# Kernel optimization log

Measured on AMD Instinct MI355X. Metric: run time of the kernel, lower is better.

The kernel has to match this reference:

```python
import jax, jax.numpy as jnp
import numpy as np

PATCHES = 196
HEADS = 12


def build_attention_mask(patches, memory_tokens_list, extension=False):
    """Additive mask: masked entries -inf, allowed entries 0. Shape (1, Sq, Skv)."""
    class_tokens = len(memory_tokens_list) + 1
    input_tokens = patches + class_tokens
    total_tokens = input_tokens + sum(memory_tokens_list)
    mask = np.zeros((1, input_tokens, total_tokens), dtype=np.float32)
    mask[:, :, patches + 1:] = -np.inf
    prev = 0
    for i, mtok in enumerate(memory_tokens_list):
        ct = patches + 1 + i
        ms = input_tokens + prev
        me = ms + mtok
        if extension:
            mask[:, ct:, ct] = 0.0
            mask[:, ct:, ms:me] = 0.0
        else:
            mask[:, ct, ct] = 0.0
            mask[:, ct, ms:me] = 0.0
        prev += mtok
    return mask


def setup_inputs() -> dict:
    key = jax.random.key(0)
    ks = jax.random.split(key, 5)
    B, Sq, D, M = 64, PATCHES + 2, 768, 8  # 1 base class token + 1 memory class token
    std = 0.02
    return {
        "hidden_states": jax.random.normal(ks[0], (B, Sq, D), jnp.float32),
        "memory": jax.random.normal(ks[1], (1, M, D), jnp.float32) * std,
        "Wq": jax.random.normal(ks[2], (D, D), jnp.float32) * std,
        "bq": jnp.zeros((D,), jnp.float32),
        "Wk": jax.random.normal(ks[3], (D, D), jnp.float32) * std,
        "bk": jnp.zeros((D,), jnp.float32),
        "Wv": jax.random.normal(ks[4], (D, D), jnp.float32) * std,
        "bv": jnp.zeros((D,), jnp.float32),
    }


def _split_heads(x, heads):
    B, S, D = x.shape
    return x.reshape(B, S, heads, D // heads)  # bshd


def reference(hidden_states, memory, Wq, bq, Wk, bk, Wv, bv):
    B, Sq, D = hidden_states.shape
    M = memory.shape[1]
    head_dim = D // HEADS
    scale = 1.0 / jnp.sqrt(jnp.asarray(head_dim, hidden_states.dtype))
    # static additive mask (1, Sq, Skv)
    mask = jnp.asarray(build_attention_mask(PATCHES, [M]))

    with_memory = jnp.concatenate(
        [hidden_states, jnp.broadcast_to(memory, (B, M, D))], axis=1)  # (B, Skv, D)

    q = _split_heads(hidden_states @ Wq + bq, HEADS)  # (B,Sq,H,dh)
    k = _split_heads(with_memory @ Wk + bk, HEADS)    # (B,Skv,H,dh)
    v = _split_heads(with_memory @ Wv + bv, HEADS)

    scores = jnp.einsum("bqhd,bkhd->bhqk", q, k) * scale + mask[:, None]  # (B,H,Sq,Skv)
    probs = jax.nn.softmax(scores, axis=-1)  # dropout is identity in eval
    ctx = jnp.einsum("bhqk,bkhd->bqhd", probs, v)
    return ctx.reshape(B, Sq, D)
```

## Files before the change

kernel.cpp:

```cpp
#include <hip/hip_runtime.h>

typedef __attribute__((ext_vector_type(8))) short bf16x8;
typedef __attribute__((ext_vector_type(4))) float f32x4;
typedef __attribute__((ext_vector_type(4))) unsigned int u32x4;

#define NB 64
#define SQ 198
#define SKV 206
#define DM 768
#define NH 12
#define NROWS (NB * SKV)
#define NCOL 2304

static __device__ __forceinline__ unsigned short f2b(float f) {
  union { float f; unsigned u; } v; v.f = f;
  unsigned r = v.u + 0x7FFFu + ((v.u >> 16) & 1u);
  return (unsigned short)(r >> 16);
}

typedef const __attribute__((address_space(1))) unsigned int g_u32;
typedef __attribute__((address_space(3))) unsigned int l_u32;
static __device__ __forceinline__ void gload_lds16(const void* g, void* l) {
  __builtin_amdgcn_global_load_lds((g_u32*)g, (l_u32*)l, 16, 0, 0);
}

__global__ __launch_bounds__(256) void k_conv_x(const float* __restrict__ hid,
                                                const float* __restrict__ mem,
                                                unsigned short* __restrict__ xkv) {
  int idx = (blockIdx.x * 256 + threadIdx.x) * 8;
  int r = idx / DM;
  int c = idx - r * DM;
  int b = r / SKV, s = r - b * SKV;
  const float* src = (s < SQ) ? (hid + (b * SQ + s) * DM + c)
                              : (mem + (s - SQ) * DM + c);
  float4 v0 = ((const float4*)src)[0];
  float4 v1 = ((const float4*)src)[1];
  unsigned w0 = f2b(v0.x) | ((unsigned)f2b(v0.y) << 16);
  unsigned w1 = f2b(v0.z) | ((unsigned)f2b(v0.w) << 16);
  unsigned w2 = f2b(v1.x) | ((unsigned)f2b(v1.y) << 16);
  unsigned w3 = f2b(v1.z) | ((unsigned)f2b(v1.w) << 16);
  u32x4 o = {w0, w1, w2, w3};
  *(u32x4*)(xkv + idx) = o;
}

__global__ __launch_bounds__(256) void k_conv_w(const float* __restrict__ Wq,
                                                const float* __restrict__ Wk,
                                                const float* __restrict__ Wv,
                                                unsigned short* __restrict__ wt) {
  __shared__ float L[64][65];
  int w = blockIdx.z;
  int n0 = blockIdx.x * 64, k0 = blockIdx.y * 64;
  const float* W = (w == 0) ? Wq : (w == 1) ? Wk : Wv;
  int tid = threadIdx.x;
#pragma unroll
  for (int i = 0; i < 16; ++i) {
    int idx = i * 256 + tid;
    int lr = idx >> 6, lc = idx & 63;
    L[lr][lc] = W[(k0 + lr) * DM + n0 + lc];
  }
  __syncthreads();
  unsigned short* dst = wt + w * DM * DM;
#pragma unroll
  for (int o = 0; o < 2; ++o) {
    int gi = o * 256 + tid;
    int rn = gi >> 3, g = gi & 7;
    unsigned wrd[4];
#pragma unroll
    for (int jj = 0; jj < 4; ++jj) {
      float f0 = L[g * 8 + jj * 2 + 0][rn];
      float f1 = L[g * 8 + jj * 2 + 1][rn];
      wrd[jj] = f2b(f0) | ((unsigned)f2b(f1) << 16);
    }
    u32x4 o4 = {wrd[0], wrd[1], wrd[2], wrd[3]};
    *(u32x4*)(dst + (n0 + rn) * DM + k0 + g * 8) = o4;
  }
}

__global__ __launch_bounds__(512, 4) void k_gemm(const unsigned short* __restrict__ xkv,
                                                 const unsigned short* __restrict__ wt,
                                                 const float* __restrict__ bq,
                                                 const float* __restrict__ bk,
                                                 const float* __restrict__ bv,
                                                 unsigned short* __restrict__ cout) {
  __shared__ __align__(16) unsigned char smem[73728];
  int o = blockIdx.x, xcd = o & 7, rest = o >> 3;
  int sid = (xcd < 7 ? xcd * 116 : 812) + (xcd < 7 ? 0 : (xcd - 7) * 115) + rest;
  int mtile = sid / 9, ntile = sid - mtile * 9;
  int row0 = mtile * 128, col0 = ntile * 256;
  int w = ntile / 3;
  int colw0 = (ntile - w * 3) * 256;
  int tid = threadIdx.x, lane = tid & 63, wid = tid >> 6;
  int wm = wid >> 2, wn = wid & 3;
  int l = lane & 15, gq = lane >> 4;
  const unsigned short* wbase = wt + w * DM * DM;

  const unsigned short* aP;
  const unsigned short* bP0;
  const unsigned short* bP1;
  {
    int sr = tid >> 2, pg = tid & 3, sg = pg ^ ((sr >> 1) & 3);
    aP  = xkv   + (row0 + sr) * DM + sg * 8;
    bP0 = wbase + (colw0 + sr) * DM + sg * 8;
    bP1 = wbase + (colw0 + 128 + sr) * DM + sg * 8;
  }
  int ldsW = wid * 1024;

  f32x4 zero = {0.f, 0.f, 0.f, 0.f};
  f32x4 acc[4][4];
#pragma unroll
  for (int i = 0; i < 4; ++i)
#pragma unroll
    for (int j = 0; j < 4; ++j) acc[i][j] = zero;

#pragma unroll
  for (int p = 0; p < 2; ++p) {
    int bo = p * 24576;
    gload_lds16(aP  + p * 32, smem + bo + ldsW);
    gload_lds16(bP0 + p * 32, smem + bo + 8192 + ldsW);
    gload_lds16(bP1 + p * 32, smem + bo + 16384 + ldsW);
  }
  asm volatile("s_waitcnt vmcnt(3)" ::: "memory");
  __builtin_amdgcn_s_barrier();

  int swx = (gq * 16) ^ (((l >> 1) & 3) << 4);
  int aRd = (wm * 64 + l) * 64 + swx;
  int bRd = 8192 + (wn * 64 + l) * 64 + swx;

  int q = 0;
  int qn = 2;
#pragma unroll 1
  for (int t = 0; t < 24; ++t) {
    const unsigned char* bp = smem + q * 24576;
    if (t < 22) {
      unsigned char* ip = smem + qn * 24576;
      int kI = (t + 2) * 32;
      gload_lds16(aP  + kI, ip + ldsW);
      gload_lds16(bP0 + kI, ip + 8192 + ldsW);
      gload_lds16(bP1 + kI, ip + 16384 + ldsW);
    }
    bf16x8 a[4], b[4];
#pragma unroll
    for (int mi = 0; mi < 4; ++mi) a[mi] = *(const bf16x8*)(bp + aRd + mi * 1024);
#pragma unroll
    for (int ni = 0; ni < 4; ++ni) b[ni] = *(const bf16x8*)(bp + bRd + ni * 1024);
    __builtin_amdgcn_s_setprio(1);
#pragma unroll
    for (int mi = 0; mi < 4; ++mi)
#pragma unroll
      for (int ni = 0; ni < 4; ++ni)
        acc[mi][ni] = __builtin_amdgcn_mfma_f32_16x16x32_bf16(a[mi], b[ni], acc[mi][ni], 0, 0, 0);
    __builtin_amdgcn_s_setprio(0);
    if (t < 22)       { asm volatile("s_waitcnt vmcnt(3)" ::: "memory"); }
    else if (t == 22) { asm volatile("s_waitcnt vmcnt(0)" ::: "memory"); }
    __builtin_amdgcn_s_barrier();
    q = (q == 2) ? 0 : q + 1;
    qn = (qn == 2) ? 0 : qn + 1;
  }

  const float* bias = (w == 0) ? bq : (w == 1) ? bk : bv;
  float bb[4];
#pragma unroll
  for (int ni = 0; ni < 4; ++ni) bb[ni] = bias[colw0 + wn * 64 + ni * 16 + l];

  __syncthreads();
#pragma unroll
  for (int mi = 0; mi < 4; ++mi)
#pragma unroll
    for (int ni = 0; ni < 4; ++ni)
#pragma unroll
      for (int rr = 0; rr < 4; ++rr) {
        int row = wm * 64 + mi * 16 + gq * 4 + rr;
        int col = wn * 64 + ni * 16 + l;
        *(unsigned short*)(smem + row * 512 + ((col * 2) ^ ((row & 7) << 4))) =
            f2b(acc[mi][ni][rr] + bb[ni]);
      }
  __syncthreads();
#pragma unroll
  for (int it = 0; it < 8; ++it) {
    int gi = it * 512 + tid;
    int row = gi >> 5, gran = gi & 31;
    u32x4 v = *(const u32x4*)(smem + row * 512 + ((gran * 16) ^ ((row & 7) << 4)));
    *(u32x4*)(cout + (row0 + row) * NCOL + col0 + gran * 8) = v;
  }
}

static __device__ __forceinline__ int vt_off(int row, int col) {
  return row * 416 + ((col * 2) ^ (((row >> 3) & 1) << 4));
}

__global__ __launch_bounds__(256, 3) void k_attn(const unsigned short* __restrict__ cqkv,
                                                 float* __restrict__ out) {
  __shared__ __align__(16) unsigned short Ksh[208 * 64];
  __shared__ __align__(16) unsigned char  VtB[64 * 416];
  int bh = blockIdx.x;
  int b = bh / NH, h = bh - b * NH;
  int tid = threadIdx.x, lane = tid & 63, wid = tid >> 6;
  int g = lane >> 4, l = lane & 15;
  const unsigned short* Cb = cqkv + (b * SKV) * NCOL + h * 64;

  if (tid < 64) *(unsigned*)(VtB + vt_off(tid, 206)) = 0u;
  for (int i = tid; i < 208 * 8; i += 256) {
    int row = i >> 3, gg = i & 7;
    int srow = (row < SKV) ? row : (SKV - 1);
    u32x4 v = *(const u32x4*)(Cb + srow * NCOL + 768 + gg * 8);
    *(u32x4*)((unsigned char*)Ksh + ((row * 128 + gg * 16) ^ ((row & 7) << 4))) = v;
  }
  for (int i = tid; i < 206 * 8; i += 256) {
    int key = i >> 3, gg = i & 7;
    u32x4 v = *(const u32x4*)(Cb + key * NCOL + 1536 + gg * 8);
    union { u32x4 v4; unsigned short e[8]; } u; u.v4 = v;
#pragma unroll
    for (int j = 0; j < 8; ++j)
      *(unsigned short*)(VtB + vt_off(gg * 8 + j, key)) = u.e[j];
  }
  __syncthreads();

  const float scale = 0.125f;
  f32x4 zero4 = {0.f, 0.f, 0.f, 0.f};
  int srcA = ((g & 1) << 5) + l;
  int srcB = srcA + 16;
  bool hiHalf = (g >= 2);

  for (int qt = wid; qt < 13; qt += 4) {
    int qr = qt * 16 + l;
    int qld = qr > 197 ? 197 : qr;
    const unsigned short* qp = Cb + qld * NCOL + g * 8;
    bf16x8 qa0 = *(const bf16x8*)qp;
    bf16x8 qa1 = *(const bf16x8*)(qp + 32);

    f32x4 sc[13];
#pragma unroll
    for (int nt = 0; nt < 13; ++nt) sc[nt] = zero4;
#pragma unroll
    for (int nt = 0; nt < 13; ++nt) {
      int key = nt * 16 + l;
      int rb = key * 128, sw = (key & 7) << 4, kb = g * 16;
      bf16x8 kb0 = *(const bf16x8*)((const unsigned char*)Ksh + rb + (kb ^ sw));
      bf16x8 kb1 = *(const bf16x8*)((const unsigned char*)Ksh + rb + ((kb + 64) ^ sw));
      sc[nt] = __builtin_amdgcn_mfma_f32_16x16x32_bf16(kb0, qa0, sc[nt], 0, 0, 0);
      sc[nt] = __builtin_amdgcn_mfma_f32_16x16x32_bf16(kb1, qa1, sc[nt], 0, 0, 0);
    }

    float mx = -1e30f;
#pragma unroll
    for (int nt = 0; nt < 13; ++nt)
#pragma unroll
      for (int r = 0; r < 4; ++r) {
        int key = nt * 16 + g * 4 + r;
        float s = sc[nt][r] * scale;
        bool ok = (key < 197 || qr == 197) && (key < SKV);
        s = ok ? s : -1e30f;
        sc[nt][r] = s;
        mx = fmaxf(mx, s);
      }
    mx = fmaxf(mx, __shfl_xor(mx, 16));
    mx = fmaxf(mx, __shfl_xor(mx, 32));
    float sum = 0.f;
#pragma unroll
    for (int nt = 0; nt < 13; ++nt)
#pragma unroll
      for (int r = 0; r < 4; ++r) {
        float p = __expf(sc[nt][r] - mx);
        sc[nt][r] = p;
        sum += p;
      }
    sum += __shfl_xor(sum, 16);
    sum += __shfl_xor(sum, 32);
    float inv = 1.0f / sum;

    unsigned pk0[13], pk1[13];
#pragma unroll
    for (int nt = 0; nt < 13; ++nt) {
      asm("v_cvt_pk_bf16_f32 %0, %1, %2" : "=v"(pk0[nt]) : "v"(sc[nt][0]), "v"(sc[nt][1]));
      asm("v_cvt_pk_bf16_f32 %0, %1, %2" : "=v"(pk1[nt]) : "v"(sc[nt][2]), "v"(sc[nt][3]));
    }

    f32x4 ctx[4];
#pragma unroll
    for (int dt = 0; dt < 4; ++dt) ctx[dt] = zero4;
#pragma unroll
    for (int c = 0; c < 7; ++c) {
      union { unsigned w[4]; bf16x8 v; } pa;
      if (c < 6) {
        int n0 = 2 * c, n1 = 2 * c + 1;
        unsigned a0 = (unsigned)__shfl((int)pk0[n0], srcA), b0 = (unsigned)__shfl((int)pk0[n1], srcA);
        unsigned a1 = (unsigned)__shfl((int)pk1[n0], srcA), b1 = (unsigned)__shfl((int)pk1[n1], srcA);
        unsigned a2 = (unsigned)__shfl((int)pk0[n0], srcB), b2 = (unsigned)__shfl((int)pk0[n1], srcB);
        unsigned a3 = (unsigned)__shfl((int)pk1[n0], srcB), b3 = (unsigned)__shfl((int)pk1[n1], srcB);
        pa.w[0] = hiHalf ? b0 : a0;
        pa.w[1] = hiHalf ? b1 : a1;
        pa.w[2] = hiHalf ? b2 : a2;
        pa.w[3] = hiHalf ? b3 : a3;
      } else {
        unsigned a0 = (unsigned)__shfl((int)pk0[12], srcA);
        unsigned a1 = (unsigned)__shfl((int)pk1[12], srcA);
        unsigned a2 = (unsigned)__shfl((int)pk0[12], srcB);
        unsigned a3 = (unsigned)__shfl((int)pk1[12], srcB);
        pa.w[0] = hiHalf ? 0u : a0;
        pa.w[1] = hiHalf ? 0u : a1;
        pa.w[2] = hiHalf ? 0u : a2;
        pa.w[3] = hiHalf ? 0u : a3;
      }
      int colb = c * 32 + g * 8;
      if (c == 6 && hiHalf) colb = 0;
#pragma unroll
      for (int dt = 0; dt < 4; ++dt) {
        bf16x8 vb = *(const bf16x8*)(VtB + vt_off(dt * 16 + l, colb));
        ctx[dt] = __builtin_amdgcn_mfma_f32_16x16x32_bf16(pa.v, vb, ctx[dt], 0, 0, 0);
      }
    }

    float invr[4];
#pragma unroll
    for (int r = 0; r < 4; ++r) invr[r] = __shfl(inv, g * 4 + r);
#pragma unroll
    for (int dt = 0; dt < 4; ++dt)
#pragma unroll
      for (int r = 0; r < 4; ++r) {
        int qo = qt * 16 + g * 4 + r;
        if (qo < SQ)
          out[(b * SQ + qo) * DM + h * 64 + dt * 16 + l] = ctx[dt][r] * invr[r];
      }
  }
}

extern "C" void kernel_launch(void* const* d_in, const int* in_sizes, int n_in,
                              void* d_out, int out_size, void* d_ws, size_t ws_size,
                              hipStream_t stream) {
  const float* hid = (const float*)d_in[0];
  const float* mem = (const float*)d_in[1];
  const float* Wq  = (const float*)d_in[2];
  const float* bq  = (const float*)d_in[3];
  const float* Wk  = (const float*)d_in[4];
  const float* bk  = (const float*)d_in[5];
  const float* Wv  = (const float*)d_in[6];
  const float* bv  = (const float*)d_in[7];
  float* out = (float*)d_out;

  unsigned short* xkv  = (unsigned short*)d_ws;
  unsigned short* wt   = xkv + NROWS * DM;
  unsigned short* cbuf = wt + 3 * DM * DM;

  k_conv_x<<<dim3(NROWS * DM / 8 / 256), 256, 0, stream>>>(hid, mem, xkv);
  k_conv_w<<<dim3(12, 12, 3), 256, 0, stream>>>(Wq, Wk, Wv, wt);
  k_gemm<<<dim3(927), 512, 0, stream>>>(xkv, wt, bq, bk, bv, cbuf);
  k_attn<<<dim3(NB * NH), 256, 0, stream>>>(cbuf, out);
}
```

Before: 103.0 us.

## Fuse fp32-to-bf16 activation conversion into GEMM A-tile loading

Removes the separate activation conversion kernel and its bf16 workspace. The GEMM now loads fp32 hidden/memory rows directly into registers, converts them with packed bf16 conversion instructions, and writes them into the swizzled LDS tile one stage ahead. This saves a kernel launch and a full write and read of the converted activation buffer. In exchange, A loads go through registers instead of direct global-to-LDS loads, fp32 doubles A-side global traffic across the nine column tiles, and the main loop gains extra wait counts.

```diff
diff --git a/kernel.cpp b/kernel.cpp
--- a/kernel.cpp
+++ b/kernel.cpp
@@ -22,25 +22,6 @@
 typedef __attribute__((address_space(3))) unsigned int l_u32;
 static __device__ __forceinline__ void gload_lds16(const void* g, void* l) {
   __builtin_amdgcn_global_load_lds((g_u32*)g, (l_u32*)l, 16, 0, 0);
-}
-
-__global__ __launch_bounds__(256) void k_conv_x(const float* __restrict__ hid,
-                                                const float* __restrict__ mem,
-                                                unsigned short* __restrict__ xkv) {
-  int idx = (blockIdx.x * 256 + threadIdx.x) * 8;
-  int r = idx / DM;
-  int c = idx - r * DM;
-  int b = r / SKV, s = r - b * SKV;
-  const float* src = (s < SQ) ? (hid + (b * SQ + s) * DM + c)
-                              : (mem + (s - SQ) * DM + c);
-  float4 v0 = ((const float4*)src)[0];
-  float4 v1 = ((const float4*)src)[1];
-  unsigned w0 = f2b(v0.x) | ((unsigned)f2b(v0.y) << 16);
-  unsigned w1 = f2b(v0.z) | ((unsigned)f2b(v0.w) << 16);
-  unsigned w2 = f2b(v1.x) | ((unsigned)f2b(v1.y) << 16);
-  unsigned w3 = f2b(v1.z) | ((unsigned)f2b(v1.w) << 16);
-  u32x4 o = {w0, w1, w2, w3};
-  *(u32x4*)(xkv + idx) = o;
 }
 
 __global__ __launch_bounds__(256) void k_conv_w(const float* __restrict__ Wq,
@@ -76,7 +57,8 @@
   }
 }
 
-__global__ __launch_bounds__(512, 4) void k_gemm(const unsigned short* __restrict__ xkv,
+__global__ __launch_bounds__(512, 4) void k_gemm(const float* __restrict__ hid,
+                                                 const float* __restrict__ mem,
                                                  const unsigned short* __restrict__ wt,
                                                  const float* __restrict__ bq,
                                                  const float* __restrict__ bk,
@@ -84,7 +66,7 @@
                                                  unsigned short* __restrict__ cout) {
   __shared__ __align__(16) unsigned char smem[73728];
   int o = blockIdx.x, xcd = o & 7, rest = o >> 3;
-  int sid = (xcd < 7 ? xcd * 116 : 812) + (xcd < 7 ? 0 : (xcd - 7) * 115) + rest;
+  int sid = (xcd < 7 ? xcd * 116 : 812 + (xcd - 7) * 115) + rest;
   int mtile = sid / 9, ntile = sid - mtile * 9;
   int row0 = mtile * 128, col0 = ntile * 256;
   int w = ntile / 3;
@@ -94,12 +76,19 @@
   int l = lane & 15, gq = lane >> 4;
   const unsigned short* wbase = wt + w * DM * DM;
 
-  const unsigned short* aP;
+  int sr = tid >> 2, pg = tid & 3;
+  const float* aF;
+  {
+    int arow = row0 + sr;
+    int ab = arow / SKV, as = arow - ab * SKV;
+    aF = (as < SQ ? hid + (size_t)(ab * SQ + as) * DM
+                  : mem + (size_t)(as - SQ) * DM) + pg * 8;
+  }
+  int aWr = sr * 64 + ((pg ^ ((sr >> 1) & 3)) << 4);
   const unsigned short* bP0;
   const unsigned short* bP1;
   {
-    int sr = tid >> 2, pg = tid & 3, sg = pg ^ ((sr >> 1) & 3);
-    aP  = xkv   + (row0 + sr) * DM + sg * 8;
+    int sg = pg ^ ((sr >> 1) & 3);
     bP0 = wbase + (colw0 + sr) * DM + sg * 8;
     bP1 = wbase + (colw0 + 128 + sr) * DM + sg * 8;
   }
@@ -112,14 +101,25 @@
 #pragma unroll
     for (int j = 0; j < 4; ++j) acc[i][j] = zero;
 
-#pragma unroll
-  for (int p = 0; p < 2; ++p) {
-    int bo = p * 24576;
-    gload_lds16(aP  + p * 32, smem + bo + ldsW);
-    gload_lds16(bP0 + p * 32, smem + bo + 8192 + ldsW);
-    gload_lds16(bP1 + p * 32, smem + bo + 16384 + ldsW);
-  }
-  asm volatile("s_waitcnt vmcnt(3)" ::: "memory");
+  float4 h0a = ((const float4*)(aF + 0))[0];
+  float4 h0b = ((const float4*)(aF + 0))[1];
+  float4 hda = ((const float4*)(aF + 32))[0];
+  float4 hdb = ((const float4*)(aF + 32))[1];
+  gload_lds16(bP0 + 0, smem + 8192 + ldsW);
+  gload_lds16(bP1 + 0, smem + 16384 + ldsW);
+  gload_lds16(bP0 + 32, smem + 24576 + 8192 + ldsW);
+  gload_lds16(bP1 + 32, smem + 24576 + 16384 + ldsW);
+  asm volatile("s_waitcnt vmcnt(0)" ::: "memory");
+  {
+    unsigned c0, c1, c2, c3;
+    asm("v_cvt_pk_bf16_f32 %0, %1, %2" : "=v"(c0) : "v"(h0a.x), "v"(h0a.y));
+    asm("v_cvt_pk_bf16_f32 %0, %1, %2" : "=v"(c1) : "v"(h0a.z), "v"(h0a.w));
+    asm("v_cvt_pk_bf16_f32 %0, %1, %2" : "=v"(c2) : "v"(h0b.x), "v"(h0b.y));
+    asm("v_cvt_pk_bf16_f32 %0, %1, %2" : "=v"(c3) : "v"(h0b.z), "v"(h0b.w));
+    u32x4 wv = {c0, c1, c2, c3};
+    *(u32x4*)(smem + aWr) = wv;
+  }
+  asm volatile("s_waitcnt lgkmcnt(0)" ::: "memory");
   __builtin_amdgcn_s_barrier();
 
   int swx = (gq * 16) ^ (((l >> 1) & 3) << 4);
@@ -128,15 +128,30 @@
 
   int q = 0;
   int qn = 2;
+  int qw = 1;
 #pragma unroll 1
   for (int t = 0; t < 24; ++t) {
     const unsigned char* bp = smem + q * 24576;
+    float4 na, nb2;
     if (t < 22) {
+      const float4* pA = (const float4*)(aF + (t + 2) * 32);
+      na = pA[0]; nb2 = pA[1];
       unsigned char* ip = smem + qn * 24576;
       int kI = (t + 2) * 32;
-      gload_lds16(aP  + kI, ip + ldsW);
       gload_lds16(bP0 + kI, ip + 8192 + ldsW);
       gload_lds16(bP1 + kI, ip + 16384 + ldsW);
+    }
+    if (t < 23) {
+      if (t < 22)       { asm volatile("s_waitcnt vmcnt(6)" ::: "memory"); }
+      else              { asm volatile("s_waitcnt vmcnt(2)" ::: "memory"); }
+      unsigned c0, c1, c2, c3;
+      asm("v_cvt_pk_bf16_f32 %0, %1, %2" : "=v"(c0) : "v"(hda.x), "v"(hda.y));
+      asm("v_cvt_pk_bf16_f32 %0, %1, %2" : "=v"(c1) : "v"(hda.z), "v"(hda.w));
+      asm("v_cvt_pk_bf16_f32 %0, %1, %2" : "=v"(c2) : "v"(hdb.x), "v"(hdb.y));
+      asm("v_cvt_pk_bf16_f32 %0, %1, %2" : "=v"(c3) : "v"(hdb.z), "v"(hdb.w));
+      u32x4 wv = {c0, c1, c2, c3};
+      *(u32x4*)(smem + qw * 24576 + aWr) = wv;
+      hda = na; hdb = nb2;
     }
     bf16x8 a[4], b[4];
 #pragma unroll
@@ -150,11 +165,13 @@
       for (int ni = 0; ni < 4; ++ni)
         acc[mi][ni] = __builtin_amdgcn_mfma_f32_16x16x32_bf16(a[mi], b[ni], acc[mi][ni], 0, 0, 0);
     __builtin_amdgcn_s_setprio(0);
-    if (t < 22)       { asm volatile("s_waitcnt vmcnt(3)" ::: "memory"); }
+    if (t < 22)       { asm volatile("s_waitcnt vmcnt(4)" ::: "memory"); }
     else if (t == 22) { asm volatile("s_waitcnt vmcnt(0)" ::: "memory"); }
+    asm volatile("s_waitcnt lgkmcnt(0)" ::: "memory");
     __builtin_amdgcn_s_barrier();
     q = (q == 2) ? 0 : q + 1;
     qn = (qn == 2) ? 0 : qn + 1;
+    qw = (qw == 2) ? 0 : qw + 1;
   }
 
   const float* bias = (w == 0) ? bq : (w == 1) ? bk : bv;
@@ -337,12 +354,10 @@
   const float* bv  = (const float*)d_in[7];
   float* out = (float*)d_out;
 
-  unsigned short* xkv  = (unsigned short*)d_ws;
-  unsigned short* wt   = xkv + NROWS * DM;
-  unsigned short* cbuf = wt + 3 * DM * DM;
-
-  k_conv_x<<<dim3(NROWS * DM / 8 / 256), 256, 0, stream>>>(hid, mem, xkv);
-  k_conv_w<<<dim3(12, 12, 3), 256, 0, stream>>>(Wq, Wk, Wv, wt);
-  k_gemm<<<dim3(927), 512, 0, stream>>>(xkv, wt, bq, bk, bv, cbuf);
+  unsigned short* wtb  = (unsigned short*)d_ws;
+  unsigned short* cbuf = wtb + 3 * DM * DM;
+
+  k_conv_w<<<dim3(12, 12, 3), 256, 0, stream>>>(Wq, Wk, Wv, wtb);
+  k_gemm<<<dim3(927), 512, 0, stream>>>(hid, mem, wtb, bq, bk, bv, cbuf);
   k_attn<<<dim3(NB * NH), 256, 0, stream>>>(cbuf, out);
 }
```

Measured after the change: 105.0 us. 1.02x slower.
